# Performance work log

Hardware: AMD Instinct MI355X
Metric: run time of the kernel (lower is better)

## Reference

```python
import jax, jax.numpy as jnp
import numpy as np

K_REGION = 32
C_CONTEXT = 128
CONF_THR = 0.5


def safe_normalize(x):
    return x / jnp.maximum(x.sum(axis=-1, keepdims=True), 1e-6)


def _geometry(mask_grid, h, w):
    # mask_grid: [B, K, h*w] -> per-mask bbox (x_min,y_min,x_max,y_max) + area, vectorized
    B, K, _ = mask_grid.shape
    m2 = mask_grid.reshape(B, K, h, w)
    present = m2 > 0.05
    rows = present.any(-1)  # [B,K,h]
    cols = present.any(-2)  # [B,K,w]
    yi = jnp.arange(h)
    xi = jnp.arange(w)
    y_min = jnp.min(jnp.where(rows, yi, h), axis=-1).astype(jnp.float32)
    y_max = jnp.max(jnp.where(rows, yi, -1), axis=-1).astype(jnp.float32)
    x_min = jnp.min(jnp.where(cols, xi, w), axis=-1).astype(jnp.float32)
    x_max = jnp.max(jnp.where(cols, xi, -1), axis=-1).astype(jnp.float32)
    hden = float(max(h - 1, 1))
    wden = float(max(w - 1, 1))
    area = present.astype(jnp.float32).mean(axis=(-1, -2))
    geom = jnp.stack([x_min / wden, y_min / hden, x_max / wden, y_max / hden, area], axis=-1)
    has_any = present.any(axis=(-1, -2))
    return jnp.where(has_any[..., None], geom, 0.0).astype(mask_grid.dtype)


def setup_inputs():
    key = jax.random.key(0)
    ks = jax.random.split(key, 16)
    B, N, D, M, Hm, Wm, Qd, Hd = 8, 576, 1024, 64, 384, 384, 4096, 1024
    inp = {}
    inp['patch_tokens'] = jax.random.normal(ks[0], (B, N, D), jnp.float32)
    inp['masks'] = jax.random.uniform(ks[1], (B, M, Hm, Wm), jnp.float32)
    inp['scores'] = jax.random.uniform(ks[2], (B, M), jnp.float32)
    inp['question_embed'] = jax.random.normal(ks[3], (B, Qd), jnp.float32)
    s = 0.02
    inp['W1'] = jax.random.normal(ks[4], (5, D), jnp.float32) * s
    inp['b1'] = jnp.zeros((D,), jnp.float32)
    inp['W2'] = jax.random.normal(ks[5], (D, D), jnp.float32) * s
    inp['b2'] = jnp.zeros((D,), jnp.float32)
    inp['Wv'] = jax.random.normal(ks[6], (D, Hd), jnp.float32) * s
    inp['bv'] = jnp.zeros((Hd,), jnp.float32)
    inp['Wp'] = jax.random.normal(ks[7], (1, Hd), jnp.float32) * s
    inp['bp'] = jnp.zeros((Hd,), jnp.float32)
    inp['Wq'] = jax.random.normal(ks[8], (Qd, Hd), jnp.float32) * s
    inp['bq'] = jnp.zeros((Hd,), jnp.float32)
    inp['Wo'] = jax.random.normal(ks[9], (Hd, 1), jnp.float32) * s
    inp['bo'] = jnp.zeros((1,), jnp.float32)
    inp['type_emb'] = jax.random.normal(ks[10], (3, D), jnp.float32) * s
    inp['patch_h'] = 24
    inp['patch_w'] = 24
    return inp


def reference(patch_tokens, masks, scores, question_embed, W1, b1, W2, b2,
              Wv, bv, Wp, bp, Wq, bq, Wo, bo, type_emb, patch_h, patch_w):
    B, N, D = patch_tokens.shape
    h, w = patch_h, patch_w
    M = masks.shape[1]

    grounding_valid = (masks.reshape(B, M, -1).sum(-1) > 0).any(-1)  # [B]

    order = jnp.argsort(-scores, axis=1)
    scores_s = jnp.take_along_axis(scores, order, axis=1)
    masks_s = jnp.take_along_axis(masks, order[:, :, None, None], axis=1)
    masks_k = masks_s[:, :K_REGION]
    scores_k = scores_s[:, :K_REGION]
    valid = scores_k >= CONF_THR
    masks_k = masks_k * valid[:, :, None, None].astype(masks_k.dtype)
    scores_k = jnp.where(valid, scores_k, 0.0)

    # MaskDownsampler: adaptive avg pool (exact: Hm,Wm divisible by h,w)
    Hm, Wm = masks_k.shape[-2:]
    fh, fw = Hm // h, Wm // w
    mg = masks_k.reshape(B, K_REGION, h, fh, w, fw).mean(axis=(3, 5)).reshape(B, K_REGION, h * w)

    uniform = jnp.full((B, K_REGION, N), 1.0 / N, dtype=patch_tokens.dtype)
    mg = jnp.where(grounding_valid[:, None, None], mg, uniform)
    scores_k = jnp.where(grounding_valid[:, None], scores_k, 1.0)

    # RegionPooler
    nm = safe_normalize(jnp.maximum(mg, 0.0))
    pooled = jnp.einsum('bkn,bnd->bkd', nm, patch_tokens)
    weighted = pooled * scores_k[..., None]
    geom = _geometry(mg, h, w)  # [B,K,5]
    g = jax.nn.silu(geom @ W1 + b1) @ W2 + b2
    region_tokens = weighted + g

    patch_prior = (mg * scores_k[..., None]).sum(axis=1)
    patch_prior = safe_normalize(jnp.maximum(patch_prior, 0.0))
    patch_prior = jnp.where(grounding_valid[:, None], patch_prior, jnp.full_like(patch_prior, 1.0 / N))

    # RoutingScorer
    hid = jnp.tanh(patch_tokens @ Wv + bv
                   + patch_prior[:, :, None] @ Wp + bp
                   + (question_embed @ Wq + bq)[:, None, :])
    routing_scores = (hid @ Wo + bo)[..., 0]  # [B,N]
    routing_weights = jax.nn.softmax(routing_scores, axis=-1)

    top_k = min(C_CONTEXT, N)
    _, sel_idx = jax.lax.top_k(routing_scores, top_k)
    context_tokens = jnp.take_along_axis(patch_tokens, sel_idx[:, :, None], axis=1)
    sel_mask = jnp.zeros((B, N), patch_tokens.dtype).at[jnp.arange(B)[:, None], sel_idx].set(1.0)

    # BackgroundPooler
    residual = jnp.maximum(1.0 - sel_mask, 0.0)
    residual = residual / jnp.maximum(residual.sum(-1, keepdims=True), 1e-6)
    bg = jnp.einsum('bn,bnd->bd', residual, patch_tokens)

    region_tokens = region_tokens + type_emb[0][None, None, :]
    context_tokens = context_tokens + type_emb[1][None, None, :]
    background_token = bg[:, None, :] + type_emb[2][None, None, :]
    visual_tokens = jnp.concatenate([region_tokens, context_tokens, background_token], axis=1)

    return (visual_tokens, region_tokens, context_tokens, background_token,
            patch_prior, routing_weights, sel_idx, grounding_valid)
```

## Files before the change

### kernel.cpp

```cpp
#include <hip/hip_runtime.h>
#include <math.h>

typedef long long I64;

#define NB    8
#define NTOK  576
#define DIM   1024
#define NMASK 64
#define HMASK 384
#define WMASK 384
#define QDIM  4096
#define HDIM  1024
#define KREG  32
#define CCTX  128
#define GH    24
#define GW    24
#define GNUM  576

#define OFF_VIS 0
#define OFF_REG 1318912
#define OFF_CTX 1581056
#define OFF_BG  2629632
#define OFF_PP  2637824
#define OFF_RW  2642432
#define OFF_SEL 2647040
#define OFF_GV  2648064

#define WS_BS   0
#define WS_NMAT 294912
#define WS_SCK  442368
#define WS_H1   442624
#define WS_Q    704768
#define WS_GV   717568
#define WS_PP   722184
#define WS_RSP  726792
#define WS_CS   763656
#define WS_Q2   771848

#define QBLK      256
#define BS_BLOCKS (NB * NMASK * 24)

__global__ __launch_bounds__(384) void k_bsq(const float* __restrict__ masks,
                                             const float* __restrict__ qe,
                                             const float* __restrict__ Wq,
                                             const float* __restrict__ bq,
                                             float* __restrict__ ws) {
  int gid = blockIdx.x;
  int t = threadIdx.x;
  __shared__ float shm[2048 + 6 * 64];
  if (gid >= QBLK) {
    int gid2 = gid - QBLK;
    int yband = gid2 % 24;
    int bm = gid2 / 24;
    float (*sm)[96] = (float(*)[96])shm;
    const float4* src = (const float4*)(masks + (I64)bm * (HMASK * WMASK) + (I64)yband * 16 * WMASK);
    float4 s4 = src[t];
    float4 v1 = src[t + 384];
    float4 v2 = src[t + 768];
    float4 v3 = src[t + 1152];
    s4.x += v1.x; s4.y += v1.y; s4.z += v1.z; s4.w += v1.w;
    s4.x += v2.x; s4.y += v2.y; s4.z += v2.z; s4.w += v2.w;
    s4.x += v3.x; s4.y += v3.y; s4.z += v3.z; s4.w += v3.w;
    float s = (s4.x + s4.y) + (s4.z + s4.w);
    sm[t / 96][t % 96] = s;
    __syncthreads();
    if (t < 24) {
      float tt = 0.f;
      #pragma unroll
      for (int rg = 0; rg < 4; ++rg)
        #pragma unroll
        for (int c = 0; c < 4; ++c) tt += sm[rg][t * 4 + c];
      ws[WS_BS + (I64)bm * GNUM + yband * 24 + t] = tt;
    }
  } else {
    int b = gid >> 5;
    int r = gid & 31;
    int qb = r >> 1;
    int ih = r & 1;
    int base = ih * 2048;
    float* qs = shm;
    float (*sp)[64] = (float(*)[64])(shm + 2048);
    {
      const float4* s4 = (const float4*)(qe + (I64)b * QDIM + base);
      float4 v = s4[t];
      *(float4*)&qs[t * 4] = v;
      if (t < 128) {
        float4 v2 = s4[t + 384];
        *(float4*)&qs[(t + 384) * 4] = v2;
      }
    }
    __syncthreads();
    int dl = t & 63, ig = t >> 6;
    int d = qb * 64 + dl;
    const float* wq = Wq + d;
    float a0 = 0.f, a1 = 0.f, a2 = 0.f, a3 = 0.f;
    int i = ig;
    for (; i + 18 < 2048; i += 24) {
      a0 = fmaf(qs[i],      wq[(I64)(base + i) * HDIM],      a0);
      a1 = fmaf(qs[i + 6],  wq[(I64)(base + i + 6) * HDIM],  a1);
      a2 = fmaf(qs[i + 12], wq[(I64)(base + i + 12) * HDIM], a2);
      a3 = fmaf(qs[i + 18], wq[(I64)(base + i + 18) * HDIM], a3);
    }
    for (; i < 2048; i += 6)
      a0 = fmaf(qs[i], wq[(I64)(base + i) * HDIM], a0);
    sp[ig][dl] = (a0 + a1) + (a2 + a3);
    __syncthreads();
    if (t < 64) {
      float s2 = ((sp[0][t] + sp[1][t]) + (sp[2][t] + sp[3][t])) + (sp[4][t] + sp[5][t]);
      int dd = qb * 64 + t;
      float outv = s2 + (ih ? 0.f : bq[dd]);
      ws[(ih ? WS_Q2 : WS_Q) + (I64)b * HDIM + dd] = outv;
    }
  }
}

#define MGPAD 580
__global__ __launch_bounds__(256) void k_perbatch(
    const float* __restrict__ bs, const float* __restrict__ scores,
    const float* __restrict__ W1, const float* __restrict__ b1,
    float* __restrict__ ws, float* __restrict__ out) {
  int b = blockIdx.x;
  int t = threadIdx.x;
  __shared__ float s_mg[KREG][MGPAD];
  __shared__ float s_sc[NMASK];
  __shared__ float s_msum[NMASK];
  __shared__ int   s_order[NMASK];
  __shared__ float s_sck[KREG];
  __shared__ int   s_valid[KREG];
  __shared__ int   s_midx[KREG];
  __shared__ float s_rowsum[KREG];
  __shared__ float s_pp[GNUM];
  __shared__ float s_geom[KREG][5];
  __shared__ float s_red[64];
  __shared__ int   s_gv;
  __shared__ float s_ppsum;

  {
    int m = t >> 2, q = t & 3;
    const float4* p = (const float4*)(bs + ((I64)b * NMASK + m) * GNUM) + q * 36;
    float s = 0.f;
    #pragma unroll 4
    for (int j = 0; j < 36; ++j) {
      float4 v = p[j];
      s += v.x; s += v.y; s += v.z; s += v.w;
    }
    s += __shfl_xor(s, 1);
    s += __shfl_xor(s, 2);
    if (q == 0) s_msum[m] = s;
  }
  if (t < NMASK) s_sc[t] = scores[b * NMASK + t];
  __syncthreads();
  if (t == 0) {
    int g = 0;
    for (int m = 0; m < NMASK; ++m) g |= (s_msum[m] > 0.f) ? 1 : 0;
    s_gv = g;
  }
  if (t < NMASK) {
    float v = s_sc[t];
    int r = 0;
    for (int j = 0; j < NMASK; ++j) {
      float vj = s_sc[j];
      r += (vj > v) || (vj == v && j < t);
    }
    s_order[r] = t;
  }
  __syncthreads();
  const int gv = s_gv;
  if (t < KREG) {
    int m = s_order[t];
    float sc = s_sc[m];
    int valid = (sc >= 0.5f) ? 1 : 0;
    s_midx[t] = m;
    s_valid[t] = valid;
    float sck = gv ? (valid ? sc : 0.f) : 1.f;
    s_sck[t] = sck;
    ws[WS_SCK + b * KREG + t] = sck;
  }
  __syncthreads();
  {
    int k = t >> 3, sub = t & 7;
    const float inv256 = 1.f / 256.f;
    const float invN = 1.f / 576.f;
    float scale = gv ? (s_valid[k] ? inv256 : 0.f) : 0.f;
    float addv  = gv ? 0.f : invN;
    const float4* src = (const float4*)(bs + ((I64)b * NMASK + s_midx[k]) * GNUM) + sub * 18;
    float* dst = &s_mg[k][sub * 72];
    #pragma unroll 3
    for (int j = 0; j < 18; ++j) {
      float4 v = src[j];
      v.x = v.x * scale + addv;
      v.y = v.y * scale + addv;
      v.z = v.z * scale + addv;
      v.w = v.w * scale + addv;
      *(float4*)(dst + j * 4) = v;
    }
  }
  __syncthreads();
  {
    int k = t >> 3, sub = t & 7;
    float part = 0.f;
    for (int n = sub; n < GNUM; n += 8) part += fmaxf(s_mg[k][n], 0.f);
    part += __shfl_xor(part, 1);
    part += __shfl_xor(part, 2);
    part += __shfl_xor(part, 4);
    if (sub == 0) s_rowsum[k] = part;
  }
  __syncthreads();
  for (int idx = t; idx < KREG * GNUM; idx += 256) {
    int k = idx / GNUM, n = idx - k * GNUM;
    float v = fmaxf(s_mg[k][n], 0.f);
    ws[WS_NMAT + ((I64)b * KREG + k) * GNUM + n] = v / fmaxf(s_rowsum[k], 1e-6f);
  }
  for (int n = t; n < GNUM; n += 256) {
    float raw = 0.f;
    #pragma unroll
    for (int k = 0; k < KREG; ++k) raw = fmaf(s_mg[k][n], s_sck[k], raw);
    s_pp[n] = fmaxf(raw, 0.f);
  }
  __syncthreads();
  if (t < 64) {
    float s = 0.f;
    for (int n = t; n < GNUM; n += 64) s += s_pp[n];
    s_red[t] = s;
  }
  __syncthreads();
  if (t == 0) {
    float s = 0.f;
    for (int i = 0; i < 64; ++i) s += s_red[i];
    s_ppsum = s;
  }
  __syncthreads();
  {
    const float invN = 1.f / 576.f;
    float den = fmaxf(s_ppsum, 1e-6f);
    for (int n = t; n < GNUM; n += 256) {
      float v = gv ? (s_pp[n] / den) : invN;
      ws[WS_PP + b * GNUM + n] = v;
      out[OFF_PP + b * GNUM + n] = v;
    }
  }
  {
    int k = t >> 3, sub = t & 7;
    unsigned colmask = 0u;
    int ymin = GH, ymax = -1, cnt = 0;
    #pragma unroll
    for (int yy = 0; yy < 3; ++yy) {
      int y = sub * 3 + yy;
      unsigned rowm = 0u;
      for (int x = 0; x < GW; ++x)
        if (s_mg[k][y * GW + x] > 0.05f) rowm |= (1u << x);
      if (rowm) { if (y < ymin) ymin = y; if (y > ymax) ymax = y; }
      colmask |= rowm;
      cnt += __popc(rowm);
    }
    #pragma unroll
    for (int off = 1; off < 8; off <<= 1) {
      colmask |= (unsigned)__shfl_xor((int)colmask, off);
      cnt += __shfl_xor(cnt, off);
      int o1 = __shfl_xor(ymin, off); ymin = (o1 < ymin) ? o1 : ymin;
      int o2 = __shfl_xor(ymax, off); ymax = (o2 > ymax) ? o2 : ymax;
    }
    if (sub == 0) {
      float g0, g1, g2, g3, g4;
      if (cnt > 0) {
        int xmin = __ffs(colmask) - 1;
        int xmax = 31 - __clz(colmask);
        g0 = (float)xmin / 23.f;
        g1 = (float)ymin / 23.f;
        g2 = (float)xmax / 23.f;
        g3 = (float)ymax / 23.f;
        g4 = (float)cnt / 576.f;
      } else { g0 = g1 = g2 = g3 = g4 = 0.f; }
      s_geom[k][0] = g0; s_geom[k][1] = g1; s_geom[k][2] = g2;
      s_geom[k][3] = g3; s_geom[k][4] = g4;
    }
  }
  __syncthreads();
  for (int idx = t; idx < KREG * HDIM; idx += 256) {
    int k = idx >> 10, j = idx & 1023;
    float x = 0.f;
    #pragma unroll
    for (int i = 0; i < 5; ++i) x += s_geom[k][i] * W1[i * HDIM + j];
    x += b1[j];
    float sg = 1.f / (1.f + expf(-x));
    ws[WS_H1 + ((I64)b * KREG + k) * HDIM + j] = x * sg;
  }
  if (t == 0) {
    float g = gv ? 1.f : 0.f;
    ws[WS_GV + b] = g;
    out[OFF_GV + b] = g;
  }
}

__global__ __launch_bounds__(512) void k_region(
    const float* __restrict__ pt, const float* __restrict__ W2,
    const float* __restrict__ b2, const float* __restrict__ te,
    float* __restrict__ ws, float* __restrict__ out) {
  int blk = blockIdx.x;
  int b = blk >> 6, kg = (blk >> 3) & 7, dg = blk & 7;
  int t = threadIdx.x;
  int dl = t & 127;
  int qh = t >> 7;
  int d = dg * 128 + dl;
  const float* nmb = ws + WS_NMAT + ((I64)b * KREG + kg * 4) * GNUM;
  const float* h1b = ws + WS_H1 + ((I64)b * KREG + kg * 4) * HDIM;
  float accP[4] = {0, 0, 0, 0};
  float accG[4] = {0, 0, 0, 0};
  float accS = 0.f;
  int n0 = qh * 144, n1 = n0 + 144;
  for (int n = n0; n < n1; ++n) {
    float p = pt[((I64)b * NTOK + n) * DIM + d];
    accS += p;
    #pragma unroll
    for (int kk = 0; kk < 4; ++kk)
      accP[kk] = fmaf(nmb[kk * GNUM + n], p, accP[kk]);
  }
  int j0 = qh * 256, j1 = j0 + 256;
  for (int j = j0; j < j1; ++j) {
    float wv = W2[(I64)j * DIM + d];
    #pragma unroll
    for (int kk = 0; kk < 4; ++kk)
      accG[kk] = fmaf(h1b[kk * HDIM + j], wv, accG[kk]);
  }
  __shared__ float cmbP[4][4][128];
  __shared__ float cmbG[4][4][128];
  __shared__ float cmbS[4][128];
  #pragma unroll
  for (int kk = 0; kk < 4; ++kk) {
    cmbP[qh][kk][dl] = accP[kk];
    cmbG[qh][kk][dl] = accG[kk];
  }
  cmbS[qh][dl] = accS;
  __syncthreads();
  if (qh == 0) {
    float bb = b2[d], t0 = te[d];
    #pragma unroll
    for (int kk = 0; kk < 4; ++kk) {
      int k = kg * 4 + kk;
      float P = (cmbP[0][kk][dl] + cmbP[1][kk][dl]) + (cmbP[2][kk][dl] + cmbP[3][kk][dl]);
      float G = (cmbG[0][kk][dl] + cmbG[1][kk][dl]) + (cmbG[2][kk][dl] + cmbG[3][kk][dl]);
      float val = P * ws[WS_SCK + b * KREG + k] + G + bb + t0;
      out[OFF_REG + ((I64)b * KREG + k) * DIM + d] = val;
      out[OFF_VIS + ((I64)b * 161 + k) * DIM + d] = val;
    }
    if (kg == 0)
      ws[WS_CS + (I64)b * DIM + d] =
          (cmbS[0][dl] + cmbS[1][dl]) + (cmbS[2][dl] + cmbS[3][dl]);
  }
}

#define BM 48
#define BN 128
#define BK 32
#define KSTEPS (DIM / BK)
__global__ __launch_bounds__(256) void k_hid2(
    const float* __restrict__ pt, const float* __restrict__ Wv,
    const float* __restrict__ bv, const float* __restrict__ Wp,
    const float* __restrict__ bp, const float* __restrict__ Wo,
    float* __restrict__ ws) {
  int blk = blockIdx.x;
  int b  = blk / 96;
  int r  = blk % 96;
  int tt = r >> 3;
  int ct = r & 7;
  int n0 = tt * BM;
  int col0 = ct * BN;
  int t = threadIdx.x;
  int tcol = t & 31;
  int trow = t >> 5;

  __shared__ float sA[2][BK][BM];
  __shared__ float sW[2][BK][BN];

  float acc[6][4];
  #pragma unroll
  for (int i = 0; i < 6; ++i)
    #pragma unroll
    for (int j = 0; j < 4; ++j) acc[i][j] = 0.f;

  int a_tok = t >> 2, a_q = t & 3;
  const I64 a_row = ((I64)b * NTOK + n0 + a_tok) * DIM;
  int w_r = t >> 3, w_c = t & 7;
  const float* w_base = Wv + (I64)w_r * HDIM + col0;

  float4 a0 = {0,0,0,0}, a1 = {0,0,0,0};
  float4 wr0, wr1, wr2, wr3;

  {
    if (t < 192) {
      a0 = *(const float4*)&pt[a_row + a_q * 8];
      a1 = *(const float4*)&pt[a_row + a_q * 8 + 4];
    }
    const float* wb = w_base;
    wr0 = *(const float4*)&wb[(w_c +  0) * 4];
    wr1 = *(const float4*)&wb[(w_c +  8) * 4];
    wr2 = *(const float4*)&wb[(w_c + 16) * 4];
    wr3 = *(const float4*)&wb[(w_c + 24) * 4];
    if (t < 192) {
      #pragma unroll
      for (int j = 0; j < 4; ++j) {
        sA[0][a_q * 8 + j][a_tok]     = ((const float*)&a0)[j];
        sA[0][a_q * 8 + 4 + j][a_tok] = ((const float*)&a1)[j];
      }
    }
    *(float4*)&sW[0][w_r][(w_c +  0) * 4] = wr0;
    *(float4*)&sW[0][w_r][(w_c +  8) * 4] = wr1;
    *(float4*)&sW[0][w_r][(w_c + 16) * 4] = wr2;
    *(float4*)&sW[0][w_r][(w_c + 24) * 4] = wr3;
  }

  for (int s = 0; s < KSTEPS; ++s) {
    __syncthreads();
    int nb = s + 1;
    if (nb < KSTEPS) {
      int k0 = nb * BK;
      if (t < 192) {
        a0 = *(const float4*)&pt[a_row + k0 + a_q * 8];
        a1 = *(const float4*)&pt[a_row + k0 + a_q * 8 + 4];
      }
      const float* wb = w_base + (I64)k0 * HDIM;
      wr0 = *(const float4*)&wb[(w_c +  0) * 4];
      wr1 = *(const float4*)&wb[(w_c +  8) * 4];
      wr2 = *(const float4*)&wb[(w_c + 16) * 4];
      wr3 = *(const float4*)&wb[(w_c + 24) * 4];
    }
    int cur = s & 1;
    #pragma unroll 4
    for (int kk = 0; kk < BK; ++kk) {
      const float* ar = &sA[cur][kk][trow * 6];
      float2 a01 = *(const float2*)ar;
      float2 a23 = *(const float2*)(ar + 2);
      float2 a45 = *(const float2*)(ar + 4);
      float4 wv4 = *(const float4*)&sW[cur][kk][tcol * 4];
      float av[6] = {a01.x, a01.y, a23.x, a23.y, a45.x, a45.y};
      float wa[4] = {wv4.x, wv4.y, wv4.z, wv4.w};
      #pragma unroll
      for (int i = 0; i < 6; ++i)
        #pragma unroll
        for (int j = 0; j < 4; ++j)
          acc[i][j] = fmaf(av[i], wa[j], acc[i][j]);
    }
    if (nb < KSTEPS) {
      int nxt = nb & 1;
      if (t < 192) {
        #pragma unroll
        for (int j = 0; j < 4; ++j) {
          sA[nxt][a_q * 8 + j][a_tok]     = ((const float*)&a0)[j];
          sA[nxt][a_q * 8 + 4 + j][a_tok] = ((const float*)&a1)[j];
        }
      }
      *(float4*)&sW[nxt][w_r][(w_c +  0) * 4] = wr0;
      *(float4*)&sW[nxt][w_r][(w_c +  8) * 4] = wr1;
      *(float4*)&sW[nxt][w_r][(w_c + 16) * 4] = wr2;
      *(float4*)&sW[nxt][w_r][(w_c + 24) * 4] = wr3;
    }
  }

  int c = col0 + tcol * 4;
  float4 bv4 = *(const float4*)&bv[c];
  float4 bp4 = *(const float4*)&bp[c];
  float4 wp4 = *(const float4*)&Wp[c];
  float4 wo4 = *(const float4*)&Wo[c];
  float4 q4a = *(const float4*)&ws[WS_Q  + (I64)b * HDIM + c];
  float4 q4b = *(const float4*)&ws[WS_Q2 + (I64)b * HDIM + c];
  float bvv[4] = {bv4.x, bv4.y, bv4.z, bv4.w};
  float bpv[4] = {bp4.x, bp4.y, bp4.z, bp4.w};
  float wpv[4] = {wp4.x, wp4.y, wp4.z, wp4.w};
  float wov[4] = {wo4.x, wo4.y, wo4.z, wo4.w};
  float qv[4]  = {q4a.x + q4b.x, q4a.y + q4b.y, q4a.z + q4b.z, q4a.w + q4b.w};
  float partial[6];
  #pragma unroll
  for (int i = 0; i < 6; ++i) {
    float ppv = ws[WS_PP + b * GNUM + n0 + trow * 6 + i];
    float s = 0.f;
    #pragma unroll
    for (int j = 0; j < 4; ++j) {
      float pre = acc[i][j] + bvv[j] + bpv[j] + qv[j] + ppv * wpv[j];
      s = fmaf(wov[j], tanhf(pre), s);
    }
    partial[i] = s;
  }
  #pragma unroll
  for (int i = 0; i < 6; ++i) {
    float p = partial[i];
    p += __shfl_xor(p, 1);
    p += __shfl_xor(p, 2);
    p += __shfl_xor(p, 4);
    p += __shfl_xor(p, 8);
    p += __shfl_xor(p, 16);
    partial[i] = p;
  }
  if (tcol == 0) {
    #pragma unroll
    for (int i = 0; i < 6; ++i)
      ws[WS_RSP + ((I64)b * NTOK + n0 + trow * 6 + i) * 8 + ct] = partial[i];
  }
}

__global__ __launch_bounds__(576) void k_soft(const float* __restrict__ bo,
                                              float* __restrict__ ws, float* __restrict__ out) {
  int b = blockIdx.x, t = threadIdx.x;
  __shared__ float s_rs[NTOK];
  __shared__ float s_w[9];
  __shared__ float s_max, s_sum;
  {
    const float* p = ws + WS_RSP + ((I64)b * NTOK + t) * 8;
    float s = bo[0];
    #pragma unroll
    for (int i = 0; i < 8; ++i) s += p[i];
    s_rs[t] = s;
  }
  __syncthreads();
  float v = s_rs[t];
  int r = 0;
  for (int j = 0; j < NTOK; ++j) {
    float vj = s_rs[j];
    r += (vj > v) || (vj == v && j < t);
  }
  float m = v;
  for (int off = 1; off < 64; off <<= 1) m = fmaxf(m, __shfl_xor(m, off));
  if ((t & 63) == 0) s_w[t >> 6] = m;
  __syncthreads();
  if (t == 0) {
    float mm = s_w[0];
    for (int i = 1; i < 9; ++i) mm = fmaxf(mm, s_w[i]);
    s_max = mm;
  }
  __syncthreads();
  float e = expf(v - s_max);
  float s = e;
  for (int off = 1; off < 64; off <<= 1) s += __shfl_xor(s, off);
  if ((t & 63) == 0) s_w[t >> 6] = s;
  __syncthreads();
  if (t == 0) {
    float ss = 0.f;
    for (int i = 0; i < 9; ++i) ss += s_w[i];
    s_sum = ss;
  }
  __syncthreads();
  out[OFF_RW + b * NTOK + t] = e / s_sum;
  if (r < CCTX) out[OFF_SEL + b * CCTX + r] = (float)t;
}

__global__ __launch_bounds__(256) void k_post(const float* __restrict__ pt, const float* __restrict__ te,
                                              const float* __restrict__ ws, const float* __restrict__ outr,
                                              float* __restrict__ out) {
  int rr = blockIdx.x, b = blockIdx.y;
  int d = threadIdx.x * 4;
  if (rr < CCTX) {
    int idx = (int)outr[OFF_SEL + b * CCTX + rr];
    float4 v = *(const float4*)&pt[((I64)b * NTOK + idx) * DIM + d];
    float4 e = *(const float4*)&te[DIM + d];
    v.x += e.x; v.y += e.y; v.z += e.z; v.w += e.w;
    *(float4*)&out[OFF_CTX + ((I64)b * CCTX + rr) * DIM + d] = v;
    *(float4*)&out[OFF_VIS + ((I64)b * 161 + KREG + rr) * DIM + d] = v;
  } else {
    float4 s = *(const float4*)&ws[WS_CS + (I64)b * DIM + d];
    for (int r = 0; r < CCTX; ++r) {
      int idx = (int)outr[OFF_SEL + b * CCTX + r];
      float4 v = *(const float4*)&pt[((I64)b * NTOK + idx) * DIM + d];
      s.x -= v.x; s.y -= v.y; s.z -= v.z; s.w -= v.w;
    }
    const float rinv = 1.f / 448.f;
    float4 e = *(const float4*)&te[2 * DIM + d];
    float4 o;
    o.x = s.x * rinv + e.x; o.y = s.y * rinv + e.y;
    o.z = s.z * rinv + e.z; o.w = s.w * rinv + e.w;
    *(float4*)&out[OFF_BG + (I64)b * DIM + d] = o;
    *(float4*)&out[OFF_VIS + ((I64)b * 161 + 160) * DIM + d] = o;
  }
}

extern "C" void kernel_launch(void* const* d_in, const int* in_sizes, int n_in,
                              void* d_out, int out_size, void* d_ws, size_t ws_size,
                              hipStream_t stream) {
  (void)in_sizes; (void)n_in; (void)out_size; (void)ws_size;
  const float* pt     = (const float*)d_in[0];
  const float* masks  = (const float*)d_in[1];
  const float* scores = (const float*)d_in[2];
  const float* qe     = (const float*)d_in[3];
  const float* W1     = (const float*)d_in[4];
  const float* b1     = (const float*)d_in[5];
  const float* W2     = (const float*)d_in[6];
  const float* b2     = (const float*)d_in[7];
  const float* Wv     = (const float*)d_in[8];
  const float* bv     = (const float*)d_in[9];
  const float* Wp     = (const float*)d_in[10];
  const float* bp     = (const float*)d_in[11];
  const float* Wq     = (const float*)d_in[12];
  const float* bq     = (const float*)d_in[13];
  const float* Wo     = (const float*)d_in[14];
  const float* bo     = (const float*)d_in[15];
  const float* te     = (const float*)d_in[16];
  float* out = (float*)d_out;
  float* ws  = (float*)d_ws;

  k_bsq<<<dim3(QBLK + BS_BLOCKS), dim3(384), 0, stream>>>(masks, qe, Wq, bq, ws);
  k_perbatch<<<dim3(NB), dim3(256), 0, stream>>>(ws + WS_BS, scores, W1, b1, ws, out);
  k_region<<<dim3(512), dim3(512), 0, stream>>>(pt, W2, b2, te, ws, out);
  k_hid2<<<dim3(768), dim3(256), 0, stream>>>(pt, Wv, bv, Wp, bp, Wo, ws);
  k_soft<<<dim3(NB), dim3(576), 0, stream>>>(bo, ws, out);
  k_post<<<dim3(CCTX + 1, NB), dim3(256), 0, stream>>>(pt, te, ws, out, out);
}
```

Baseline: 375.6 us.

## Restructure routing GEMM to read Wv directly and widen Wq unroll

The routing hidden GEMM is rewritten with a new tiling of 64 tokens by 64 columns. The Wv tile is no longer staged in shared memory; each wave reads 16 columns of Wv straight from global memory as a uniform broadcast, while each lane keeps one token held in shared memory. The partial-score layout grows to 16 column tiles per token, and the softmax kernel now reads these with float4 loads. The question projection loop is also unrolled to eight accumulators for more memory-level parallelism. The GEMM relies on cache hits for Wv reads and does less register blocking per thread, which could reduce FMA efficiency.

```diff
diff --git a/kernel.cpp b/kernel.cpp
--- a/kernel.cpp
+++ b/kernel.cpp
@@ -31,11 +31,11 @@
 #define WS_SCK  442368
 #define WS_H1   442624
 #define WS_Q    704768
-#define WS_GV   717568
-#define WS_PP   722184
-#define WS_RSP  726792
-#define WS_CS   763656
-#define WS_Q2   771848
+#define WS_Q2   712960
+#define WS_GV   721152
+#define WS_PP   721160
+#define WS_CS   725768
+#define WS_RSP  733960
 
 #define QBLK      256
 #define BS_BLOCKS (NB * NMASK * 24)
@@ -94,16 +94,21 @@
     int d = qb * 64 + dl;
     const float* wq = Wq + d;
     float a0 = 0.f, a1 = 0.f, a2 = 0.f, a3 = 0.f;
+    float a4 = 0.f, a5 = 0.f, a6 = 0.f, a7 = 0.f;
     int i = ig;
-    for (; i + 18 < 2048; i += 24) {
+    for (; i + 42 < 2048; i += 48) {
       a0 = fmaf(qs[i],      wq[(I64)(base + i) * HDIM],      a0);
       a1 = fmaf(qs[i + 6],  wq[(I64)(base + i + 6) * HDIM],  a1);
       a2 = fmaf(qs[i + 12], wq[(I64)(base + i + 12) * HDIM], a2);
       a3 = fmaf(qs[i + 18], wq[(I64)(base + i + 18) * HDIM], a3);
+      a4 = fmaf(qs[i + 24], wq[(I64)(base + i + 24) * HDIM], a4);
+      a5 = fmaf(qs[i + 30], wq[(I64)(base + i + 30) * HDIM], a5);
+      a6 = fmaf(qs[i + 36], wq[(I64)(base + i + 36) * HDIM], a6);
+      a7 = fmaf(qs[i + 42], wq[(I64)(base + i + 42) * HDIM], a7);
     }
     for (; i < 2048; i += 6)
       a0 = fmaf(qs[i], wq[(I64)(base + i) * HDIM], a0);
-    sp[ig][dl] = (a0 + a1) + (a2 + a3);
+    sp[ig][dl] = ((a0 + a1) + (a2 + a3)) + ((a4 + a5) + (a6 + a7));
     __syncthreads();
     if (t < 64) {
       float s2 = ((sp[0][t] + sp[1][t]) + (sp[2][t] + sp[3][t])) + (sp[4][t] + sp[5][t]);
@@ -349,151 +354,114 @@
   }
 }
 
-#define BM 48
-#define BN 128
-#define BK 32
-#define KSTEPS (DIM / BK)
-__global__ __launch_bounds__(256) void k_hid2(
+__global__ __launch_bounds__(256) void k_hid3(
     const float* __restrict__ pt, const float* __restrict__ Wv,
     const float* __restrict__ bv, const float* __restrict__ Wp,
     const float* __restrict__ bp, const float* __restrict__ Wo,
     float* __restrict__ ws) {
   int blk = blockIdx.x;
-  int b  = blk / 96;
-  int r  = blk % 96;
-  int tt = r >> 3;
-  int ct = r & 7;
-  int n0 = tt * BM;
-  int col0 = ct * BN;
+  int b = blk / 144;
+  int r = blk % 144;
+  int tokTile = r >> 4;
+  int colTile = r & 15;
+  int n0 = tokTile * 64;
   int t = threadIdx.x;
-  int tcol = t & 31;
-  int trow = t >> 5;
-
-  __shared__ float sA[2][BK][BM];
-  __shared__ float sW[2][BK][BN];
-
-  float acc[6][4];
+  int wv = t >> 6;
+  int lane = t & 63;
+  int col0 = colTile * 64 + wv * 16;
+
+  __shared__ float sA[2][32][64];
+  __shared__ float s_part[4][64];
+
+  float acc[16];
   #pragma unroll
-  for (int i = 0; i < 6; ++i)
-    #pragma unroll
-    for (int j = 0; j < 4; ++j) acc[i][j] = 0.f;
-
-  int a_tok = t >> 2, a_q = t & 3;
-  const I64 a_row = ((I64)b * NTOK + n0 + a_tok) * DIM;
-  int w_r = t >> 3, w_c = t & 7;
-  const float* w_base = Wv + (I64)w_r * HDIM + col0;
-
-  float4 a0 = {0,0,0,0}, a1 = {0,0,0,0};
-  float4 wr0, wr1, wr2, wr3;
-
-  {
-    if (t < 192) {
-      a0 = *(const float4*)&pt[a_row + a_q * 8];
-      a1 = *(const float4*)&pt[a_row + a_q * 8 + 4];
-    }
-    const float* wb = w_base;
-    wr0 = *(const float4*)&wb[(w_c +  0) * 4];
-    wr1 = *(const float4*)&wb[(w_c +  8) * 4];
-    wr2 = *(const float4*)&wb[(w_c + 16) * 4];
-    wr3 = *(const float4*)&wb[(w_c + 24) * 4];
-    if (t < 192) {
+  for (int j = 0; j < 16; ++j) acc[j] = 0.f;
+
+  int kq = t & 7;
+  int tokp = t >> 3;
+  const I64 rowbase0 = ((I64)b * NTOK + n0 + tokp) * DIM;
+  const I64 rowbase1 = ((I64)b * NTOK + n0 + tokp + 32) * DIM;
+
+  float4 r0 = *(const float4*)&pt[rowbase0 + kq * 4];
+  float4 r1 = *(const float4*)&pt[rowbase1 + kq * 4];
+  #pragma unroll
+  for (int i = 0; i < 4; ++i) {
+    sA[0][kq * 4 + i][tokp]      = ((const float*)&r0)[i];
+    sA[0][kq * 4 + i][tokp + 32] = ((const float*)&r1)[i];
+  }
+
+  const float* wbase = Wv + col0;
+  for (int s = 0; s < 32; ++s) {
+    __syncthreads();
+    if (s + 1 < 32) {
+      int k0n = (s + 1) * 32;
+      r0 = *(const float4*)&pt[rowbase0 + k0n + kq * 4];
+      r1 = *(const float4*)&pt[rowbase1 + k0n + kq * 4];
+    }
+    int cur = s & 1;
+    int k0 = s * 32;
+    #pragma unroll 4
+    for (int kk = 0; kk < 32; ++kk) {
+      float av = sA[cur][kk][lane];
+      const float* wr = wbase + (I64)(k0 + kk) * HDIM;
+      float4 w0 = *(const float4*)(wr);
+      float4 w1 = *(const float4*)(wr + 4);
+      float4 w2 = *(const float4*)(wr + 8);
+      float4 w3 = *(const float4*)(wr + 12);
+      acc[0]  = fmaf(av, w0.x, acc[0]);
+      acc[1]  = fmaf(av, w0.y, acc[1]);
+      acc[2]  = fmaf(av, w0.z, acc[2]);
+      acc[3]  = fmaf(av, w0.w, acc[3]);
+      acc[4]  = fmaf(av, w1.x, acc[4]);
+      acc[5]  = fmaf(av, w1.y, acc[5]);
+      acc[6]  = fmaf(av, w1.z, acc[6]);
+      acc[7]  = fmaf(av, w1.w, acc[7]);
+      acc[8]  = fmaf(av, w2.x, acc[8]);
+      acc[9]  = fmaf(av, w2.y, acc[9]);
+      acc[10] = fmaf(av, w2.z, acc[10]);
+      acc[11] = fmaf(av, w2.w, acc[11]);
+      acc[12] = fmaf(av, w3.x, acc[12]);
+      acc[13] = fmaf(av, w3.y, acc[13]);
+      acc[14] = fmaf(av, w3.z, acc[14]);
+      acc[15] = fmaf(av, w3.w, acc[15]);
+    }
+    if (s + 1 < 32) {
+      int nxt = (s + 1) & 1;
       #pragma unroll
-      for (int j = 0; j < 4; ++j) {
-        sA[0][a_q * 8 + j][a_tok]     = ((const float*)&a0)[j];
-        sA[0][a_q * 8 + 4 + j][a_tok] = ((const float*)&a1)[j];
+      for (int i = 0; i < 4; ++i) {
+        sA[nxt][kq * 4 + i][tokp]      = ((const float*)&r0)[i];
+        sA[nxt][kq * 4 + i][tokp + 32] = ((const float*)&r1)[i];
       }
     }
-    *(float4*)&sW[0][w_r][(w_c +  0) * 4] = wr0;
-    *(float4*)&sW[0][w_r][(w_c +  8) * 4] = wr1;
-    *(float4*)&sW[0][w_r][(w_c + 16) * 4] = wr2;
-    *(float4*)&sW[0][w_r][(w_c + 24) * 4] = wr3;
-  }
-
-  for (int s = 0; s < KSTEPS; ++s) {
-    __syncthreads();
-    int nb = s + 1;
-    if (nb < KSTEPS) {
-      int k0 = nb * BK;
-      if (t < 192) {
-        a0 = *(const float4*)&pt[a_row + k0 + a_q * 8];
-        a1 = *(const float4*)&pt[a_row + k0 + a_q * 8 + 4];
-      }
-      const float* wb = w_base + (I64)k0 * HDIM;
-      wr0 = *(const float4*)&wb[(w_c +  0) * 4];
-      wr1 = *(const float4*)&wb[(w_c +  8) * 4];
-      wr2 = *(const float4*)&wb[(w_c + 16) * 4];
-      wr3 = *(const float4*)&wb[(w_c + 24) * 4];
-    }
-    int cur = s & 1;
-    #pragma unroll 4
-    for (int kk = 0; kk < BK; ++kk) {
-      const float* ar = &sA[cur][kk][trow * 6];
-      float2 a01 = *(const float2*)ar;
-      float2 a23 = *(const float2*)(ar + 2);
-      float2 a45 = *(const float2*)(ar + 4);
-      float4 wv4 = *(const float4*)&sW[cur][kk][tcol * 4];
-      float av[6] = {a01.x, a01.y, a23.x, a23.y, a45.x, a45.y};
-      float wa[4] = {wv4.x, wv4.y, wv4.z, wv4.w};
-      #pragma unroll
-      for (int i = 0; i < 6; ++i)
-        #pragma unroll
-        for (int j = 0; j < 4; ++j)
-          acc[i][j] = fmaf(av[i], wa[j], acc[i][j]);
-    }
-    if (nb < KSTEPS) {
-      int nxt = nb & 1;
-      if (t < 192) {
-        #pragma unroll
-        for (int j = 0; j < 4; ++j) {
-          sA[nxt][a_q * 8 + j][a_tok]     = ((const float*)&a0)[j];
-          sA[nxt][a_q * 8 + 4 + j][a_tok] = ((const float*)&a1)[j];
-        }
-      }
-      *(float4*)&sW[nxt][w_r][(w_c +  0) * 4] = wr0;
-      *(float4*)&sW[nxt][w_r][(w_c +  8) * 4] = wr1;
-      *(float4*)&sW[nxt][w_r][(w_c + 16) * 4] = wr2;
-      *(float4*)&sW[nxt][w_r][(w_c + 24) * 4] = wr3;
-    }
-  }
-
-  int c = col0 + tcol * 4;
-  float4 bv4 = *(const float4*)&bv[c];
-  float4 bp4 = *(const float4*)&bp[c];
-  float4 wp4 = *(const float4*)&Wp[c];
-  float4 wo4 = *(const float4*)&Wo[c];
-  float4 q4a = *(const float4*)&ws[WS_Q  + (I64)b * HDIM + c];
-  float4 q4b = *(const float4*)&ws[WS_Q2 + (I64)b * HDIM + c];
-  float bvv[4] = {bv4.x, bv4.y, bv4.z, bv4.w};
-  float bpv[4] = {bp4.x, bp4.y, bp4.z, bp4.w};
-  float wpv[4] = {wp4.x, wp4.y, wp4.z, wp4.w};
-  float wov[4] = {wo4.x, wo4.y, wo4.z, wo4.w};
-  float qv[4]  = {q4a.x + q4b.x, q4a.y + q4b.y, q4a.z + q4b.z, q4a.w + q4b.w};
-  float partial[6];
+  }
+
+  float ppv = ws[WS_PP + b * GNUM + n0 + lane];
+  float ssum = 0.f;
   #pragma unroll
-  for (int i = 0; i < 6; ++i) {
-    float ppv = ws[WS_PP + b * GNUM + n0 + trow * 6 + i];
-    float s = 0.f;
-    #pragma unroll
-    for (int j = 0; j < 4; ++j) {
-      float pre = acc[i][j] + bvv[j] + bpv[j] + qv[j] + ppv * wpv[j];
-      s = fmaf(wov[j], tanhf(pre), s);
-    }
-    partial[i] = s;
-  }
-  #pragma unroll
-  for (int i = 0; i < 6; ++i) {
-    float p = partial[i];
-    p += __shfl_xor(p, 1);
-    p += __shfl_xor(p, 2);
-    p += __shfl_xor(p, 4);
-    p += __shfl_xor(p, 8);
-    p += __shfl_xor(p, 16);
-    partial[i] = p;
-  }
-  if (tcol == 0) {
-    #pragma unroll
-    for (int i = 0; i < 6; ++i)
-      ws[WS_RSP + ((I64)b * NTOK + n0 + trow * 6 + i) * 8 + ct] = partial[i];
+  for (int jj = 0; jj < 4; ++jj) {
+    int c = col0 + jj * 4;
+    float4 bv4 = *(const float4*)&bv[c];
+    float4 bp4 = *(const float4*)&bp[c];
+    float4 wp4 = *(const float4*)&Wp[c];
+    float4 wo4 = *(const float4*)&Wo[c];
+    float4 qa  = *(const float4*)&ws[WS_Q  + (I64)b * HDIM + c];
+    float4 qb  = *(const float4*)&ws[WS_Q2 + (I64)b * HDIM + c];
+    float bvv[4] = {bv4.x, bv4.y, bv4.z, bv4.w};
+    float bpv[4] = {bp4.x, bp4.y, bp4.z, bp4.w};
+    float wpv[4] = {wp4.x, wp4.y, wp4.z, wp4.w};
+    float wov[4] = {wo4.x, wo4.y, wo4.z, wo4.w};
+    float qv[4]  = {qa.x + qb.x, qa.y + qb.y, qa.z + qb.z, qa.w + qb.w};
+    #pragma unroll
+    for (int e = 0; e < 4; ++e) {
+      float pre = acc[jj * 4 + e] + bvv[e] + bpv[e] + qv[e] + ppv * wpv[e];
+      ssum = fmaf(wov[e], tanhf(pre), ssum);
+    }
+  }
+  s_part[wv][lane] = ssum;
+  __syncthreads();
+  if (wv == 0) {
+    float tot = (s_part[0][lane] + s_part[1][lane]) + (s_part[2][lane] + s_part[3][lane]);
+    ws[WS_RSP + ((I64)b * NTOK + n0 + lane) * 16 + colTile] = tot;
   }
 }
 
@@ -504,10 +472,13 @@
   __shared__ float s_w[9];
   __shared__ float s_max, s_sum;
   {
-    const float* p = ws + WS_RSP + ((I64)b * NTOK + t) * 8;
+    const float4* p = (const float4*)(ws + WS_RSP + ((I64)b * NTOK + t) * 16);
     float s = bo[0];
     #pragma unroll
-    for (int i = 0; i < 8; ++i) s += p[i];
+    for (int i = 0; i < 4; ++i) {
+      float4 v = p[i];
+      s += (v.x + v.y) + (v.z + v.w);
+    }
     s_rs[t] = s;
   }
   __syncthreads();
@@ -598,7 +569,7 @@
   k_bsq<<<dim3(QBLK + BS_BLOCKS), dim3(384), 0, stream>>>(masks, qe, Wq, bq, ws);
   k_perbatch<<<dim3(NB), dim3(256), 0, stream>>>(ws + WS_BS, scores, W1, b1, ws, out);
   k_region<<<dim3(512), dim3(512), 0, stream>>>(pt, W2, b2, te, ws, out);
-  k_hid2<<<dim3(768), dim3(256), 0, stream>>>(pt, Wv, bv, Wp, bp, Wo, ws);
+  k_hid3<<<dim3(1152), dim3(256), 0, stream>>>(pt, Wv, bv, Wp, bp, Wo, ws);
   k_soft<<<dim3(NB), dim3(576), 0, stream>>>(bo, ws, out);
   k_post<<<dim3(CCTX + 1, NB), dim3(256), 0, stream>>>(pt, te, ws, out, out);
 }
```

Result: slower. 795.7 us (+111.8%).
